# Performance work log

Measured on AMD Instinct MI355X. Metric: run time of the kernel, lower is better.

## Reference

```python
import jax, jax.numpy as jnp
import numpy as np

NEG = -1000000000.0

def _gru(x, h, W_ih, W_hh, b_ih, b_hh):
    # torch GRUCell semantics; W_ih: [3H, H_in], W_hh: [3H, H]
    gi = x @ W_ih.T + b_ih
    gh = h @ W_hh.T + b_hh
    i_r, i_z, i_n = jnp.split(gi, 3, axis=-1)
    h_r, h_z, h_n = jnp.split(gh, 3, axis=-1)
    r = jax.nn.sigmoid(i_r + h_r)
    z = jax.nn.sigmoid(i_z + h_z)
    n = jnp.tanh(i_n + r * h_n)
    return (1.0 - z) * n + z * h

def setup_inputs():
    key = jax.random.key(0)
    ks = jax.random.split(key, 32)
    N, E, ND, ED, H, P, L, M, S = 50000, 800000, 16, 16, 128, 16, 8, 6, 320
    sc = 0.05
    inp = {}
    inp['node_feat'] = jax.random.normal(ks[0], (N, ND), jnp.float32)
    inp['edge_feat'] = jax.random.normal(ks[1], (E, ED), jnp.float32)
    inp['edge_index'] = jax.random.randint(ks[2], (2, E), 0, N)
    inp['paths'] = jax.random.randint(ks[3], (P, L), 0, E)
    inp['path_mask'] = jnp.ones((P,), jnp.int32)
    inp['path_features'] = jax.random.normal(ks[4], (P, 3), jnp.float32)
    inp['mod_masks'] = jnp.ones((P, M), jnp.int32)
    inp['spec_masks'] = jnp.ones((P, M, S), jnp.int32)
    inp['path_spectrum'] = jax.random.uniform(ks[5], (P, S), jnp.float32)
    # parameters
    inp['W_np'] = jax.random.normal(ks[6], (ND, H), jnp.float32) * sc
    inp['b_np'] = jnp.zeros((H,), jnp.float32)
    inp['W_ep'] = jax.random.normal(ks[7], (ED, H), jnp.float32) * sc
    inp['b_ep'] = jnp.zeros((H,), jnp.float32)
    inp['W_msg'] = jax.random.normal(ks[8], (2 * H, H), jnp.float32) * sc
    inp['b_msg'] = jnp.zeros((H,), jnp.float32)
    inp['W_ih'] = jax.random.normal(ks[9], (3 * H, H), jnp.float32) * sc
    inp['b_ih'] = jnp.zeros((3 * H,), jnp.float32)
    inp['W_hh'] = jax.random.normal(ks[10], (3 * H, H), jnp.float32) * sc
    inp['b_hh'] = jnp.zeros((3 * H,), jnp.float32)
    inp['W_path'] = jax.random.normal(ks[11], (H, 1), jnp.float32) * sc
    inp['b_path'] = jnp.zeros((1,), jnp.float32)
    inp['W_mod'] = jax.random.normal(ks[12], (H + 3, M), jnp.float32) * sc
    inp['b_mod'] = jnp.zeros((M,), jnp.float32)
    inp['conv1_w'] = jax.random.normal(ks[13], (8, 1, 5), jnp.float32) * sc
    inp['conv1_b'] = jnp.zeros((8,), jnp.float32)
    inp['conv2_w'] = jax.random.normal(ks[14], (1, 8, 1), jnp.float32) * sc
    inp['conv2_b'] = jnp.zeros((1,), jnp.float32)
    inp['W_val'] = jax.random.normal(ks[15], (H, 1), jnp.float32) * sc
    inp['b_val'] = jnp.zeros((1,), jnp.float32)
    return inp

def reference(node_feat, edge_feat, edge_index, paths, path_mask, path_features,
              mod_masks, spec_masks, path_spectrum,
              W_np, b_np, W_ep, b_ep, W_msg, b_msg, W_ih, b_ih, W_hh, b_hh,
              W_path, b_path, W_mod, b_mod, conv1_w, conv1_b, conv2_w, conv2_b,
              W_val, b_val):
    N = node_feat.shape[0]
    # --- GNN encoder (3 iterations of gather -> message -> scatter -> GRU) ---
    h = node_feat @ W_np + b_np                       # [N, H]
    e = edge_feat @ W_ep + b_ep                       # [E, H]
    src, dst = edge_index[0], edge_index[1]
    for _ in range(3):
        m = jnp.concatenate([h[src], e], axis=-1) @ W_msg + b_msg   # [E, H]
        agg = jax.ops.segment_sum(m, dst, num_segments=N)           # index_add
        h = _gru(agg, h, W_ih, W_hh, b_ih, b_hh)
    # --- value head ---
    g = h.mean(axis=0)
    value = (g @ W_val + b_val).squeeze()
    # --- path agent (deterministic=True -> argmax) ---
    z = e[paths].mean(axis=1)                         # [P, H]
    logits_p = (z @ W_path + b_path).squeeze(-1)      # [P]
    logits_p = jnp.where(path_mask == 0, NEG, logits_p)
    p = jnp.argmax(logits_p)
    logp_p = jax.nn.log_softmax(logits_p)[p]
    z_p = z[p]
    # --- modulation agent ---
    x_m = jnp.concatenate([z_p, path_features[p]], axis=-1)
    logits_m = x_m @ W_mod + b_mod                    # [M]
    logits_m = jnp.where(mod_masks[p] == 0, NEG, logits_m)
    m_sel = jnp.argmax(logits_m)
    logp_m = jax.nn.log_softmax(logits_m)[m_sel]
    # --- spectrum agent ---
    spec = path_spectrum[p][None, None, :]            # [1,1,S]
    h1 = jax.nn.relu(jax.lax.conv_general_dilated(
        spec, conv1_w, (1,), [(2, 2)], dimension_numbers=('NCH', 'OIH', 'NCH'))
        + conv1_b[None, :, None])
    h2 = jax.lax.conv_general_dilated(
        h1, conv2_w, (1,), [(0, 0)], dimension_numbers=('NCH', 'OIH', 'NCH'))
    logits_f = h2.squeeze() + conv2_b[0]
    logits_f = jnp.where(spec_masks[p, m_sel] == 0, NEG, logits_f)
    f = jnp.argmax(logits_f)
    logp_f = jax.nn.log_softmax(logits_f)[f]
    logprob = logp_p + logp_m + logp_f
    return (p, f, m_sel, logprob, value)
```

## Files before the change

kernel.cpp:

```cpp
#include <hip/hip_runtime.h>
#include <math.h>

#define NN 50000
#define NE 800000
#define HD 128
#define FD 16
#define NPATH 16
#define PL 8
#define NM 6
#define NS 320
#define NB 196
#define NSB 782
#define AK 320
#define AKU 160
#define AK1 64
#define EPB 2048
#define NBLK 391
#define NBKT 196
#define NEGV -1000000000.0f

typedef unsigned int uint;
typedef unsigned short ushort;
typedef short bf16x8 __attribute__((ext_vector_type(8)));
typedef float f32x4 __attribute__((ext_vector_type(4)));

__device__ __forceinline__ float frcp(float x){ return __builtin_amdgcn_rcpf(x); }
__device__ __forceinline__ float fsigm(float x){ return frcp(1.0f + __expf(-x)); }
__device__ __forceinline__ float ftanh(float x){ return 1.0f - 2.0f*frcp(__expf(2.0f*x) + 1.0f); }

__device__ __forceinline__ ushort f2b(float f){
    union{float f; uint u;} v; v.f=f;
    uint r = v.u + 0x7FFFu + ((v.u>>16)&1u);
    return (ushort)(r>>16);
}
__device__ __forceinline__ float b2f(ushort s){
    union{uint u; float f;} v; v.u = ((uint)s)<<16; return v.f;
}
__device__ __forceinline__ float blo(uint v){ return b2f((ushort)(v&0xFFFF)); }
__device__ __forceinline__ float bhi(uint v){ return b2f((ushort)(v>>16)); }
__device__ __forceinline__ uint pack2(float a, float b){ return (uint)f2b(a) | (((uint)f2b(b))<<16); }

__global__ void k_deg(const int* __restrict__ ei, int* __restrict__ deg){
    int e = blockIdx.x*256 + threadIdx.x;
    if (e >= NE) return;
    atomicAdd(&deg[ei[NE + e]], 1);
}

__global__ void k_scan1(const int* __restrict__ deg, int* __restrict__ offs, int* __restrict__ bsum){
    int tid = threadIdx.x, bid = blockIdx.x;
    int idx = bid*256 + tid;
    int v = (idx<NN) ? deg[idx] : 0;
    int lane = tid&63, w = tid>>6;
    int x = v;
    #pragma unroll
    for (int d=1; d<64; d<<=1){ int y = __shfl_up(x,d); if (lane>=d) x += y; }
    __shared__ int wsum[4];
    if (lane==63) wsum[w] = x;
    __syncthreads();
    int base = 0;
    #pragma unroll
    for (int j=0;j<4;j++) if (j<w) base += wsum[j];
    if (idx<NN) offs[idx] = base + x - v;
    if (tid==255) bsum[bid] = base + x;
}
__global__ void k_scan2(int* __restrict__ bsum, int* __restrict__ offs){
    int tid = threadIdx.x;
    int v = (tid<NB) ? bsum[tid] : 0;
    int lane = tid&63, w = tid>>6;
    int x = v;
    #pragma unroll
    for (int d=1; d<64; d<<=1){ int y = __shfl_up(x,d); if (lane>=d) x += y; }
    __shared__ int wsum[4];
    if (lane==63) wsum[w] = x;
    __syncthreads();
    int base = 0;
    #pragma unroll
    for (int j=0;j<4;j++) if (j<w) base += wsum[j];
    if (tid<NB) bsum[tid] = base + x - v;
    if (tid==255) offs[NN] = base + x;
}
__global__ void k_scan3(const int* __restrict__ bsum, int* __restrict__ offs){
    int idx = blockIdx.x*256 + threadIdx.x;
    if (idx>=NN) return;
    offs[idx] += bsum[blockIdx.x];
}

__global__ void k_hist(const int* __restrict__ ei, int* __restrict__ C){
    __shared__ int h[NBKT];
    int tid = threadIdx.x, blk = blockIdx.x;
    if (tid < NBKT) h[tid] = 0;
    __syncthreads();
    int e0 = blk*EPB;
    for (int i=tid; i<EPB; i+=256){
        int e = e0+i;
        if (e < NE) atomicAdd(&h[ei[NE+e]>>8], 1);
    }
    __syncthreads();
    if (tid < NBKT) C[blk*NBKT + tid] = h[tid];
}

__global__ void k_cscan(int* __restrict__ C, const int* __restrict__ offs){
    int b = blockIdx.x*4 + (threadIdx.x>>6);
    int lane = threadIdx.x & 63;
    if (b >= NBKT) return;
    int base = offs[b<<8];
    int carry = 0;
    for (int c=0; c<7; ++c){
        int i = c*64 + lane;
        int v = (i<NBLK)? C[i*NBKT + b] : 0;
        int x = v;
        #pragma unroll
        for (int d=1; d<64; d<<=1){ int y = __shfl_up(x,d); if (lane>=d) x += y; }
        if (i<NBLK) C[i*NBKT + b] = base + carry + (x - v);
        carry += __shfl(x, 63);
    }
}

__global__ void k_scatA(const int* __restrict__ ei, const int* __restrict__ C,
                        int2* __restrict__ bkt2){
    __shared__ int cur[NBKT];
    __shared__ int cbase[NBKT];
    int tid = threadIdx.x, blk = blockIdx.x;
    if (tid < NBKT){ cur[tid] = 0; cbase[tid] = C[blk*NBKT + tid]; }
    __syncthreads();
    int e0 = blk*EPB;
    for (int i=tid; i<EPB; i+=256){
        int e = e0+i;
        if (e >= NE) break;
        int dst = ei[NE+e];
        int bkt = dst>>8;
        int r = atomicAdd(&cur[bkt], 1);
        bkt2[cbase[bkt] + r] = make_int2(dst, e);
    }
}

__global__ void k_scatB(const int* __restrict__ ei, const int2* __restrict__ bkt2,
                        const int* __restrict__ offs, int2* __restrict__ csr2){
    __shared__ int cur[256];
    int b = blockIdx.x, tid = threadIdx.x;
    int d0 = b<<8;
    {
        int idx = d0 + tid;
        cur[tid] = (idx<NN)? offs[idx] : 0;
    }
    __syncthreads();
    int lo = offs[d0];
    int hi = (d0+256 <= NN)? offs[d0+256] : offs[NN];
    for (int i=lo+tid; i<hi; i+=256){
        int2 p = bkt2[i];
        int pos = atomicAdd(&cur[p.x & 255], 1);
        csr2[pos] = make_int2(ei[p.y], p.y);
    }
}

__global__ void k_gat16(const int2* __restrict__ csr2,
                        const float* __restrict__ edge_feat, const float* __restrict__ nf,
                        const int* __restrict__ offs,
                        float* __restrict__ ef_sum, float* __restrict__ nf_sum){
    int node = blockIdx.x*4 + (threadIdx.x>>6);
    int lane = threadIdx.x & 63;
    int k = lane & 15, sub = lane >> 4;
    int b = offs[node], e2 = offs[node+1];
    float ae = 0.f, an = 0.f;
    int i = b + sub;
    for (; i + 4 < e2; i += 8){
        int2 p0 = csr2[i], p1 = csr2[i+4];
        float f0 = edge_feat[(size_t)p0.y*FD + k];
        float g0 = nf[(size_t)p0.x*FD + k];
        float f1 = edge_feat[(size_t)p1.y*FD + k];
        float g1 = nf[(size_t)p1.x*FD + k];
        ae += f0 + f1; an += g0 + g1;
    }
    if (i < e2){
        int2 p0 = csr2[i];
        ae += edge_feat[(size_t)p0.y*FD + k];
        an += nf[(size_t)p0.x*FD + k];
    }
    ae += __shfl_xor(ae, 16); ae += __shfl_xor(ae, 32);
    an += __shfl_xor(an, 16); an += __shfl_xor(an, 32);
    if (sub == 0){ ef_sum[node*FD + k] = ae; nf_sum[node*FD + k] = an; }
}

__global__ void k_folds(const float* __restrict__ W_ep, const float* __restrict__ b_ep,
                        const float* __restrict__ W_msg, const float* __restrict__ b_msg,
                        float* __restrict__ Wf, float* __restrict__ bfv){
    int o = blockIdx.x*256 + threadIdx.x;
    if (o < FD*HD){
        int k=o>>7, c=o&127;
        float acc=0.f;
        for (int m=0;m<HD;m++) acc += W_ep[k*HD+m]*W_msg[(HD+m)*HD+c];
        Wf[o]=acc;
    } else if (o < FD*HD+HD){
        int c=o-FD*HD;
        float acc=b_msg[c];
        for (int m=0;m<HD;m++) acc += b_ep[m]*W_msg[(HD+m)*HD+c];
        bfv[c]=acc;
    }
}

__global__ void k_wprep2(const float* __restrict__ W_ih, const float* __restrict__ W_hh,
                         const float* __restrict__ W_msg, const float* __restrict__ Wf,
                         const float* __restrict__ bfv,
                         const float* __restrict__ b_ih, const float* __restrict__ b_hh,
                         ushort* __restrict__ W2T, float* __restrict__ Wt32){
    int c = blockIdx.x;
    int k = threadIdx.x;
    int j = c>>2, g = c&3;
    float v = 0.f;
    if (k < 128){
        float acc = 0.f;
        if (g < 3){
            const float* wm = W_msg + (size_t)k*HD;
            const float* wi = W_ih + (size_t)(g*HD+j)*HD;
            for (int m=0;m<HD;m++) acc += wm[m]*wi[m];
        }
        Wt32[(size_t)c*HD + k] = acc;
        v = acc;
    } else if (k < 256){
        int kk = k-128;
        if (g==0)      v = W_hh[(size_t)j*HD+kk];
        else if (g==1) v = W_hh[(size_t)(HD+j)*HD+kk];
        else if (g==3) v = W_hh[(size_t)(2*HD+j)*HD+kk];
    } else if (k < 272){
        if (g < 3){
            const float* wf = Wf + (size_t)(k-256)*HD;
            const float* wi = W_ih + (size_t)(g*HD+j)*HD;
            float acc=0.f;
            for (int m=0;m<HD;m++) acc += wf[m]*wi[m];
            v = acc;
        }
    } else if (k == 272){
        if (g < 3){
            const float* wi = W_ih + (size_t)(g*HD+j)*HD;
            float acc=0.f;
            for (int m=0;m<HD;m++) acc += bfv[m]*wi[m];
            v = acc;
        }
    } else if (k == 273){
        v = (g==0)? b_ih[j]+b_hh[j] : (g==1)? b_ih[HD+j]+b_hh[HD+j]
          : (g==2)? b_ih[2*HD+j] : b_hh[2*HD+j];
    }
    W2T[(size_t)c*AK + k] = f2b(v);
}

__global__ void k_wprep1(const float* __restrict__ W_np, const float* __restrict__ b_np,
                         const float* __restrict__ W_hh, const float* __restrict__ Wt32,
                         const ushort* __restrict__ W2T, ushort* __restrict__ W1T){
    int c = blockIdx.x;
    int k = threadIdx.x;
    int j = c>>2, g = c&3;
    float v = 0.f;
    if (k < 16){
        if (g != 2){
            int gp = (g==3)? 2 : g;
            const float* wh = W_hh + (size_t)(gp*HD + j)*HD;
            const float* wn = W_np + (size_t)k*HD;
            float acc=0.f;
            for (int m=0;m<HD;m++) acc += wn[m]*wh[m];
            v = acc;
        }
    } else if (k < 32){
        const float* wt = Wt32 + (size_t)c*HD;
        const float* wn = W_np + (size_t)(k-16)*HD;
        float acc=0.f;
        for (int m=0;m<HD;m++) acc += wn[m]*wt[m];
        v = acc;
    } else if (k < 48){
        v = b2f(W2T[(size_t)c*AK + 256 + (k-32)]);
    } else if (k == 48){
        float acc = b2f(W2T[(size_t)c*AK + 272]);
        const float* wt = Wt32 + (size_t)c*HD;
        for (int m=0;m<HD;m++) acc += b_np[m]*wt[m];
        v = acc;
    } else if (k == 49){
        float acc = b2f(W2T[(size_t)c*AK + 273]);
        if (g != 2){
            int gp = (g==3)? 2 : g;
            const float* wh = W_hh + (size_t)(gp*HD + j)*HD;
            for (int m=0;m<HD;m++) acc += b_np[m]*wh[m];
        }
        v = acc;
    }
    W1T[(size_t)c*AK1 + k] = f2b(v);
}

__global__ void k_prep2(const float* __restrict__ nf, const float* __restrict__ nf_sum,
                        const float* __restrict__ ef_sum, const int* __restrict__ deg,
                        ushort* __restrict__ A1p, ushort* __restrict__ A){
    int idx = blockIdx.x*256 + threadIdx.x;
    int n = idx>>5, c2 = idx&31;
    int k = c2*2, k1 = k+1;
    float d = (float)deg[n];
    float v0 = (k<16)? nf[n*FD+k] : (k<32)? nf_sum[n*FD+k-16] : (k<48)? ef_sum[n*FD+k-32]
             : (k==48)? d : 0.f;
    float v1 = (k1<16)? nf[n*FD+k1] : (k1<32)? nf_sum[n*FD+k1-16] : (k1<48)? ef_sum[n*FD+k1-32]
             : (k1==49)? 1.f : 0.f;
    ((uint*)A1p)[(size_t)n*32 + c2] = pack2(v0,v1);
    int col = 256 + k;
    float s0 = (col<272)? ef_sum[n*FD + col-256] : (col==272)? d : 0.f;
    float s1 = (col+1<272)? ef_sum[n*FD + col+1-256] : (col+1==273)? 1.f : 0.f;
    ((uint*)A)[(size_t)n*AKU + 128 + c2] = pack2(s0,s1);
}

template<bool IT1>
__global__ __launch_bounds__(256) void k_fused(const ushort* __restrict__ Asrc,
                                               const ushort* __restrict__ Bt,
                                               const float* __restrict__ nf,
                                               const float* __restrict__ W_np,
                                               const float* __restrict__ b_np,
                                               ushort* __restrict__ Ah){
    __shared__ __align__(16) short LDS[128*128];
    __shared__ float Wnp_s[FD][32];
    short* As = LDS;
    short* Bs = LDS + 128*64;
    const int tid = threadIdx.x;
    const int lane = tid & 63, w = tid>>6;
    const int wm = w>>1, wn = w&1;
    const int n0 = blockIdx.x*128, m0 = blockIdx.y*128;
    const int jbase = n0>>2;
    const int AKA = IT1 ? AK1 : AK;
    if (IT1){
        for (int i=tid; i<FD*32; i+=256){
            int kk=i>>5, jj=i&31;
            Wnp_s[kk][jj] = W_np[kk*HD + jbase + jj];
        }
    }
    f32x4 acc[4][4] = {};
    const int nsteps = IT1 ? 1 : 5;
    for (int kk=0; kk<nsteps; ++kk){
        __syncthreads();
        #pragma unroll
        for (int i=0;i<4;i++){
            int id = tid + i*256;
            int row = id>>3, s = id&7;
            int phys = row*64 + ((s ^ (row&7))<<3);
            int ar = m0 + row; if (ar >= NN) ar = NN-1;
            *(int4*)&As[phys] = *(const int4*)(Asrc + (size_t)ar*AKA + kk*64 + s*8);
            *(int4*)&Bs[phys] = *(const int4*)(Bt + (size_t)(n0+row)*AKA + kk*64 + s*8);
        }
        __syncthreads();
        #pragma unroll
        for (int ksel=0; ksel<2; ++ksel){
            bf16x8 af[4], bfr[4];
            #pragma unroll
            for (int t=0;t<4;t++){
                int arow = wm*64 + t*16 + (lane&15);
                int aslot = (ksel*4 + (lane>>4)) ^ (arow&7);
                af[t] = *(const bf16x8*)&As[arow*64 + aslot*8];
                int brow = wn*64 + t*16 + (lane&15);
                int bslot = (ksel*4 + (lane>>4)) ^ (brow&7);
                bfr[t] = *(const bf16x8*)&Bs[brow*64 + bslot*8];
            }
            #pragma unroll
            for (int mi=0;mi<4;mi++)
                #pragma unroll
                for (int ni=0;ni<4;ni++)
                    acc[mi][ni] = __builtin_amdgcn_mfma_f32_16x16x32_bf16(af[mi], bfr[ni], acc[mi][ni], 0,0,0);
        }
    }
    __syncthreads();
    #pragma unroll
    for (int mi=0;mi<4;mi++){
        #pragma unroll
        for (int ni=0;ni<4;ni++){
            #pragma unroll
            for (int r=0;r<4;r++){
                int row = wm*64 + mi*16 + (lane>>4)*4 + r;
                int col = wn*64 + ni*16 + (lane&15);
                int pc = (col&3) | (((col>>2) ^ (row&7))<<2);
                LDS[row*128 + pc] = (short)f2b(acc[mi][ni][r]);
            }
        }
    }
    __syncthreads();
    {
        int jp = tid&15, rg = tid>>4;
        int jg = jbase + jp*2;
        #pragma unroll
        for (int rr=0; rr<8; ++rr){
            int row = rg*8 + rr;
            int n = m0 + row;
            if (n >= NN) continue;
            uint2 g0 = *(const uint2*)&LDS[row*128 + (((jp*2)   ^ (row&7))<<2)];
            uint2 g1 = *(const uint2*)&LDS[row*128 + (((jp*2+1) ^ (row&7))<<2)];
            float ha, hb;
            if constexpr (IT1){
                const float* x = nf + (size_t)n*FD;
                float a = b_np[jg], b = b_np[jg+1];
                #pragma unroll
                for (int k=0;k<FD;k++){
                    float xv = x[k];
                    a += xv*Wnp_s[k][jp*2];
                    b += xv*Wnp_s[k][jp*2+1];
                }
                ha = a; hb = b;
            } else {
                uint vh = ((const uint*)Ah)[(size_t)n*AKU + 64 + (n0>>3) + jp];
                ha = blo(vh); hb = bhi(vh);
            }
            float r0 = fsigm(blo(g0.x)), z0 = fsigm(bhi(g0.x));
            float nn0 = ftanh(blo(g0.y) + r0*bhi(g0.y));
            float r1 = fsigm(blo(g1.x)), z1 = fsigm(bhi(g1.x));
            float nn1 = ftanh(blo(g1.y) + r1*bhi(g1.y));
            float h0 = (1.f-z0)*nn0 + z0*ha;
            float h1 = (1.f-z1)*nn1 + z1*hb;
            ((uint*)Ah)[(size_t)n*AKU + 64 + (n0>>3) + jp] = pack2(h0,h1);
        }
    }
}

__global__ void k_gather(ushort* __restrict__ A, const int* __restrict__ offs,
                         const int2* __restrict__ csr2){
    int node = blockIdx.x*4 + (threadIdx.x>>6);
    int c2 = threadIdx.x & 63;
    int b = offs[node], e2 = offs[node+1];
    float a0 = 0.f, a1 = 0.f;
    const uint* hp = (const uint*)A;
    int i = b;
    for (; i + 8 <= e2; i += 8){
        int s0=csr2[i].x,  s1=csr2[i+1].x, s2=csr2[i+2].x, s3=csr2[i+3].x;
        int s4=csr2[i+4].x,s5=csr2[i+5].x, s6=csr2[i+6].x, s7=csr2[i+7].x;
        uint v0=hp[(size_t)s0*AKU+64+c2], v1=hp[(size_t)s1*AKU+64+c2],
             v2=hp[(size_t)s2*AKU+64+c2], v3=hp[(size_t)s3*AKU+64+c2],
             v4=hp[(size_t)s4*AKU+64+c2], v5=hp[(size_t)s5*AKU+64+c2],
             v6=hp[(size_t)s6*AKU+64+c2], v7=hp[(size_t)s7*AKU+64+c2];
        a0 += blo(v0)+blo(v1)+blo(v2)+blo(v3)+blo(v4)+blo(v5)+blo(v6)+blo(v7);
        a1 += bhi(v0)+bhi(v1)+bhi(v2)+bhi(v3)+bhi(v4)+bhi(v5)+bhi(v6)+bhi(v7);
    }
    if (i + 4 <= e2){
        int s0=csr2[i].x,s1=csr2[i+1].x,s2=csr2[i+2].x,s3=csr2[i+3].x;
        uint v0=hp[(size_t)s0*AKU+64+c2], v1=hp[(size_t)s1*AKU+64+c2],
             v2=hp[(size_t)s2*AKU+64+c2], v3=hp[(size_t)s3*AKU+64+c2];
        a0 += blo(v0)+blo(v1)+blo(v2)+blo(v3);
        a1 += bhi(v0)+bhi(v1)+bhi(v2)+bhi(v3);
        i += 4;
    }
    for (; i < e2; ++i){
        uint v = hp[(size_t)csr2[i].x*AKU+64+c2];
        a0 += blo(v); a1 += bhi(v);
    }
    ((uint*)A)[(size_t)node*AKU + c2] = pack2(a0,a1);
}

__global__ void k_sum1(const ushort* __restrict__ A, float* __restrict__ partial){
    int bid = blockIdx.x, tid = threadIdx.x;
    int lane = tid&63, w2 = tid>>6;
    int nb = bid*64;
    float a0=0.f, a1=0.f;
    const uint* hp = (const uint*)A;
    #pragma unroll
    for (int r=w2; r<64; r+=4){
        int n = nb + r;
        if (n < NN){
            uint v = hp[(size_t)n*AKU + 64 + lane];
            a0 += blo(v); a1 += bhi(v);
        }
    }
    __shared__ float s0[4][64], s1[4][64];
    s0[w2][lane]=a0; s1[w2][lane]=a1;
    __syncthreads();
    if (w2==0){
        a0 = s0[0][lane]+s0[1][lane]+s0[2][lane]+s0[3][lane];
        a1 = s1[0][lane]+s1[1][lane]+s1[2][lane]+s1[3][lane];
        ((float2*)partial)[(size_t)bid*64 + lane] = make_float2(a0,a1);
    }
}
__global__ void k_sum2(const float* __restrict__ partial, float* __restrict__ gsum){
    int c = blockIdx.x;
    int tid = threadIdx.x;
    int lane = tid&63, w = tid>>6;
    float a = 0.f;
    for (int b=tid; b<NSB; b+=256) a += partial[(size_t)b*128 + c];
    #pragma unroll
    for (int d=1; d<64; d<<=1) a += __shfl_xor(a, d);
    __shared__ float sh[4];
    if (lane==0) sh[w]=a;
    __syncthreads();
    if (tid==0) gsum[c] = sh[0]+sh[1]+sh[2]+sh[3];
}

__global__ void k_small(const float* __restrict__ ef, const int* __restrict__ paths,
                        const int* __restrict__ pmask, const float* __restrict__ pfeat,
                        const int* __restrict__ mmask, const int* __restrict__ smask,
                        const float* __restrict__ pspec,
                        const float* __restrict__ W_ep, const float* __restrict__ b_ep,
                        const float* __restrict__ W_path, const float* __restrict__ b_path,
                        const float* __restrict__ W_mod, const float* __restrict__ b_mod,
                        const float* __restrict__ c1w, const float* __restrict__ c1b,
                        const float* __restrict__ c2w, const float* __restrict__ c2b,
                        const float* __restrict__ W_val, const float* __restrict__ b_val,
                        const float* __restrict__ gsum, float* __restrict__ out){
    __shared__ float Wep_s[FD][HD];
    __shared__ float esum[NPATH][FD];
    __shared__ float z[NPATH][HD];
    __shared__ float lf[NS];
    __shared__ float spec[NS];
    __shared__ float red[8];
    __shared__ float scal[3];
    __shared__ int   sel[3];
    __shared__ float maxsh;
    int tid = threadIdx.x, lane = tid&63, w = tid>>6;

    for (int i=tid; i<FD*HD; i+=512) Wep_s[i>>7][i&127] = W_ep[i];
    if (tid < NPATH*FD){
        int p = tid>>4, k = tid&15;
        float a = 0.f;
        #pragma unroll
        for (int l=0;l<PL;l++){
            int eid = paths[p*PL + l];
            a += ef[(size_t)eid*FD + k];
        }
        esum[p][k] = a*0.125f;
    }
    __syncthreads();
    #pragma unroll
    for (int i=tid; i<NPATH*HD; i+=512){
        int p = i>>7, c = i&127;
        float a = b_ep[c];
        #pragma unroll
        for (int k=0;k<FD;k++) a += esum[p][k]*Wep_s[k][c];
        z[p][c] = a;
    }
    __syncthreads();
    {
        int p = tid>>5, sub = tid&31;
        float part = 0.f;
        #pragma unroll
        for (int c=sub;c<HD;c+=32) part += z[p][c]*W_path[c];
        #pragma unroll
        for (int d=16; d>=1; d>>=1) part += __shfl_xor(part, d);
        if (sub==0) lf[p] = (pmask[p]==0)? NEGV : part + b_path[0];
    }
    __syncthreads();
    if (w==0){
        float v = (lane<NPATH)? lf[lane] : -3.0e38f;
        float m = v;
        #pragma unroll
        for (int d=1; d<64; d<<=1) m = fmaxf(m, __shfl_xor(m, d));
        float e = (lane<NPATH)? __expf(v-m) : 0.f;
        #pragma unroll
        for (int d=1; d<64; d<<=1) e += __shfl_xor(e, d);
        int idx = (lane<NPATH && v==m)? lane : (1<<30);
        #pragma unroll
        for (int d=1; d<64; d<<=1) idx = min(idx, __shfl_xor(idx, d));
        if (lane==0){ sel[0]=idx; scal[0] = -logf(e); }
    }
    __syncthreads();
    int pstar = sel[0];
    if (w < NM){
        float part = 0.f;
        #pragma unroll
        for (int c=lane;c<HD;c+=64) part += z[pstar][c]*W_mod[c*NM + w];
        if (lane<3) part += pfeat[pstar*3+lane]*W_mod[(HD+lane)*NM + w];
        #pragma unroll
        for (int d=1; d<64; d<<=1) part += __shfl_xor(part, d);
        if (lane==0) red[w] = (mmask[pstar*NM + w]==0)? NEGV : part + b_mod[w];
    } else if (w == 7){
        float part = gsum[lane]*W_val[lane] + gsum[lane+64]*W_val[lane+64];
        #pragma unroll
        for (int d=1; d<64; d<<=1) part += __shfl_xor(part, d);
        if (lane==0) scal[2] = part/(float)NN + b_val[0];
    }
    __syncthreads();
    if (w==0){
        float v = (lane<NM)? red[lane] : -3.0e38f;
        float m = v;
        #pragma unroll
        for (int d=1; d<64; d<<=1) m = fmaxf(m, __shfl_xor(m, d));
        float e = (lane<NM)? __expf(v-m) : 0.f;
        #pragma unroll
        for (int d=1; d<64; d<<=1) e += __shfl_xor(e, d);
        int idx = (lane<NM && v==m)? lane : (1<<30);
        #pragma unroll
        for (int d=1; d<64; d<<=1) idx = min(idx, __shfl_xor(idx, d));
        if (lane==0){ sel[1]=idx; scal[1] = -logf(e); }
    }
    __syncthreads();
    int mstar = sel[1];
    if (tid < NS) spec[tid] = pspec[pstar*NS + tid];
    __syncthreads();
    float v = -3.0e38f;
    if (tid < NS){
        float acc = c2b[0];
        #pragma unroll
        for (int ch=0; ch<8; ch++){
            float a = c1b[ch];
            #pragma unroll
            for (int k=0;k<5;k++){
                int ss = tid + k - 2;
                if (ss>=0 && ss<NS) a += spec[ss]*c1w[ch*5+k];
            }
            a = fmaxf(a, 0.f);
            acc += a*c2w[ch];
        }
        v = (smask[pstar*NM*NS + mstar*NS + tid]==0) ? NEGV : acc;
    }
    float m = v;
    #pragma unroll
    for (int d=1; d<64; d<<=1) m = fmaxf(m, __shfl_xor(m, d));
    if (lane==0) red[w] = m;
    __syncthreads();
    if (tid==0){
        float mm = red[0];
        #pragma unroll
        for (int i=1;i<8;i++) mm = fmaxf(mm, red[i]);
        maxsh = mm; sel[2] = 1<<30;
    }
    __syncthreads();
    float M2 = maxsh;
    if (tid<NS && v==M2) atomicMin(&sel[2], tid);
    float e = (tid<NS)? __expf(v-M2) : 0.f;
    #pragma unroll
    for (int d=1; d<64; d<<=1) e += __shfl_xor(e, d);
    if (lane==0) red[w] = e;
    __syncthreads();
    if (tid==0){
        float se = 0.f;
        #pragma unroll
        for (int i=0;i<8;i++) se += red[i];
        out[0] = (float)pstar;
        out[1] = (float)sel[2];
        out[2] = (float)mstar;
        out[3] = scal[0] + scal[1] - logf(se);
        out[4] = scal[2];
    }
}

extern "C" void kernel_launch(void* const* d_in, const int* in_sizes, int n_in,
                              void* d_out, int out_size, void* d_ws, size_t ws_size,
                              hipStream_t stream) {
    (void)in_sizes; (void)n_in; (void)out_size; (void)ws_size;
    const float* node_feat     = (const float*)d_in[0];
    const float* edge_feat     = (const float*)d_in[1];
    const int*   edge_index    = (const int*)d_in[2];
    const int*   paths         = (const int*)d_in[3];
    const int*   path_mask     = (const int*)d_in[4];
    const float* path_features = (const float*)d_in[5];
    const int*   mod_masks     = (const int*)d_in[6];
    const int*   spec_masks    = (const int*)d_in[7];
    const float* path_spectrum = (const float*)d_in[8];
    const float* W_np  = (const float*)d_in[9];
    const float* b_np  = (const float*)d_in[10];
    const float* W_ep  = (const float*)d_in[11];
    const float* b_ep  = (const float*)d_in[12];
    const float* W_msg = (const float*)d_in[13];
    const float* b_msg = (const float*)d_in[14];
    const float* W_ih  = (const float*)d_in[15];
    const float* b_ih  = (const float*)d_in[16];
    const float* W_hh  = (const float*)d_in[17];
    const float* b_hh  = (const float*)d_in[18];
    const float* W_path = (const float*)d_in[19];
    const float* b_path = (const float*)d_in[20];
    const float* W_mod  = (const float*)d_in[21];
    const float* b_mod  = (const float*)d_in[22];
    const float* c1w = (const float*)d_in[23];
    const float* c1b = (const float*)d_in[24];
    const float* c2w = (const float*)d_in[25];
    const float* c2b = (const float*)d_in[26];
    const float* W_val = (const float*)d_in[27];
    const float* b_val = (const float*)d_in[28];

    char* ws = (char*)d_ws;
    size_t off = 0;
    auto alloc = [&](size_t bytes)->char*{
        char* p = ws + off;
        off += (bytes + 255) & ~(size_t)255;
        return p;
    };
    int*    deg     = (int*)alloc((size_t)NN*4);
    int*    offs    = (int*)alloc((size_t)(NN+1)*4);
    int*    bsum    = (int*)alloc((size_t)NB*4);
    int*    Cmat    = (int*)alloc((size_t)NBLK*NBKT*4);
    int2*   bkt2    = (int2*)alloc((size_t)NE*8);
    int2*   csr2    = (int2*)alloc((size_t)NE*8);
    float*  ef_sum  = (float*)alloc((size_t)NN*FD*4);
    float*  nf_sum  = (float*)alloc((size_t)NN*FD*4);
    float*  Wf      = (float*)alloc((size_t)FD*HD*4);
    float*  bfv     = (float*)alloc((size_t)HD*4);
    ushort* W2T     = (ushort*)alloc((size_t)512*AK*2);
    float*  Wt32    = (float*)alloc((size_t)512*HD*4);
    ushort* W1T     = (ushort*)alloc((size_t)512*AK1*2);
    ushort* A       = (ushort*)alloc((size_t)NN*AK*2);
    ushort* A1p     = (ushort*)alloc((size_t)NN*AK1*2);
    float*  partial = (float*)alloc((size_t)NSB*HD*4);
    float*  gsum    = (float*)alloc((size_t)HD*4);

    hipMemsetAsync(deg, 0, (size_t)NN*4, stream);

    k_deg<<<(NE+255)/256, 256, 0, stream>>>(edge_index, deg);
    k_scan1<<<NB, 256, 0, stream>>>(deg, offs, bsum);
    k_scan2<<<1, 256, 0, stream>>>(bsum, offs);
    k_scan3<<<NB, 256, 0, stream>>>(bsum, offs);
    k_hist<<<NBLK, 256, 0, stream>>>(edge_index, Cmat);
    k_cscan<<<(NBKT+3)/4, 256, 0, stream>>>(Cmat, offs);
    k_scatA<<<NBLK, 256, 0, stream>>>(edge_index, Cmat, bkt2);
    k_scatB<<<NBKT, 256, 0, stream>>>(edge_index, bkt2, offs, csr2);
    k_gat16<<<NN/4, 256, 0, stream>>>(csr2, edge_feat, node_feat, offs, ef_sum, nf_sum);
    k_folds<<<9, 256, 0, stream>>>(W_ep, b_ep, W_msg, b_msg, Wf, bfv);
    k_wprep2<<<512, AK, 0, stream>>>(W_ih, W_hh, W_msg, Wf, bfv, b_ih, b_hh, W2T, Wt32);
    k_wprep1<<<512, AK1, 0, stream>>>(W_np, b_np, W_hh, Wt32, W2T, W1T);
    k_prep2<<<NN*32/256, 256, 0, stream>>>(node_feat, nf_sum, ef_sum, deg, A1p, A);

    const int MB = (NN+127)/128;
    k_fused<true><<<dim3(4,MB), 256, 0, stream>>>(A1p, W1T, node_feat, W_np, b_np, A);
    k_gather<<<NN/4, 256, 0, stream>>>(A, offs, csr2);
    k_fused<false><<<dim3(4,MB), 256, 0, stream>>>(A, W2T, node_feat, W_np, b_np, A);
    k_gather<<<NN/4, 256, 0, stream>>>(A, offs, csr2);
    k_fused<false><<<dim3(4,MB), 256, 0, stream>>>(A, W2T, node_feat, W_np, b_np, A);

    k_sum1<<<NSB, 256, 0, stream>>>(A, partial);
    k_sum2<<<HD, 256, 0, stream>>>(partial, gsum);
    k_small<<<1, 512, 0, stream>>>(edge_feat, paths, path_mask, path_features,
                                   mod_masks, spec_masks, path_spectrum,
                                   W_ep, b_ep, W_path, b_path, W_mod, b_mod,
                                   c1w, c1b, c2w, c2b, W_val, b_val,
                                   gsum, (float*)d_out);
}
```

Before: 317.2 us.

## Derive CSR offsets from bucket sort, drop degree pass, remap GEMM blocks per XCD

```diff
diff --git a/kernel.cpp b/kernel.cpp
--- a/kernel.cpp
+++ b/kernel.cpp
@@ -1,4 +1,5 @@
 #include <hip/hip_runtime.h>
+#include <hip/hip_bf16.h>
 #include <math.h>
 
 #define NN 50000
@@ -9,7 +10,6 @@
 #define PL 8
 #define NM 6
 #define NS 320
-#define NB 196
 #define NSB 782
 #define AK 320
 #define AKU 160
@@ -17,6 +17,7 @@
 #define EPB 2048
 #define NBLK 391
 #define NBKT 196
+#define MBT 391
 #define NEGV -1000000000.0f
 
 typedef unsigned int uint;
@@ -29,9 +30,9 @@
 __device__ __forceinline__ float ftanh(float x){ return 1.0f - 2.0f*frcp(__expf(2.0f*x) + 1.0f); }
 
 __device__ __forceinline__ ushort f2b(float f){
-    union{float f; uint u;} v; v.f=f;
-    uint r = v.u + 0x7FFFu + ((v.u>>16)&1u);
-    return (ushort)(r>>16);
+    union { __hip_bfloat16 h; ushort u; } v;
+    v.h = __float2bfloat16(f);
+    return v.u;
 }
 __device__ __forceinline__ float b2f(ushort s){
     union{uint u; float f;} v; v.u = ((uint)s)<<16; return v.f;
@@ -39,51 +40,6 @@
 __device__ __forceinline__ float blo(uint v){ return b2f((ushort)(v&0xFFFF)); }
 __device__ __forceinline__ float bhi(uint v){ return b2f((ushort)(v>>16)); }
 __device__ __forceinline__ uint pack2(float a, float b){ return (uint)f2b(a) | (((uint)f2b(b))<<16); }
-
-__global__ void k_deg(const int* __restrict__ ei, int* __restrict__ deg){
-    int e = blockIdx.x*256 + threadIdx.x;
-    if (e >= NE) return;
-    atomicAdd(&deg[ei[NE + e]], 1);
-}
-
-__global__ void k_scan1(const int* __restrict__ deg, int* __restrict__ offs, int* __restrict__ bsum){
-    int tid = threadIdx.x, bid = blockIdx.x;
-    int idx = bid*256 + tid;
-    int v = (idx<NN) ? deg[idx] : 0;
-    int lane = tid&63, w = tid>>6;
-    int x = v;
-    #pragma unroll
-    for (int d=1; d<64; d<<=1){ int y = __shfl_up(x,d); if (lane>=d) x += y; }
-    __shared__ int wsum[4];
-    if (lane==63) wsum[w] = x;
-    __syncthreads();
-    int base = 0;
-    #pragma unroll
-    for (int j=0;j<4;j++) if (j<w) base += wsum[j];
-    if (idx<NN) offs[idx] = base + x - v;
-    if (tid==255) bsum[bid] = base + x;
-}
-__global__ void k_scan2(int* __restrict__ bsum, int* __restrict__ offs){
-    int tid = threadIdx.x;
-    int v = (tid<NB) ? bsum[tid] : 0;
-    int lane = tid&63, w = tid>>6;
-    int x = v;
-    #pragma unroll
-    for (int d=1; d<64; d<<=1){ int y = __shfl_up(x,d); if (lane>=d) x += y; }
-    __shared__ int wsum[4];
-    if (lane==63) wsum[w] = x;
-    __syncthreads();
-    int base = 0;
-    #pragma unroll
-    for (int j=0;j<4;j++) if (j<w) base += wsum[j];
-    if (tid<NB) bsum[tid] = base + x - v;
-    if (tid==255) offs[NN] = base + x;
-}
-__global__ void k_scan3(const int* __restrict__ bsum, int* __restrict__ offs){
-    int idx = blockIdx.x*256 + threadIdx.x;
-    if (idx>=NN) return;
-    offs[idx] += bsum[blockIdx.x];
-}
 
 __global__ void k_hist(const int* __restrict__ ei, int* __restrict__ C){
     __shared__ int h[NBKT];
@@ -99,11 +55,10 @@
     if (tid < NBKT) C[blk*NBKT + tid] = h[tid];
 }
 
-__global__ void k_cscan(int* __restrict__ C, const int* __restrict__ offs){
+__global__ void k_cscanA(int* __restrict__ C, int* __restrict__ bkttot){
     int b = blockIdx.x*4 + (threadIdx.x>>6);
     int lane = threadIdx.x & 63;
     if (b >= NBKT) return;
-    int base = offs[b<<8];
     int carry = 0;
     for (int c=0; c<7; ++c){
         int i = c*64 + lane;
@@ -111,17 +66,36 @@
         int x = v;
         #pragma unroll
         for (int d=1; d<64; d<<=1){ int y = __shfl_up(x,d); if (lane>=d) x += y; }
-        if (i<NBLK) C[i*NBKT + b] = base + carry + (x - v);
+        if (i<NBLK) C[i*NBKT + b] = carry + (x - v);
         carry += __shfl(x, 63);
     }
+    if (lane==0) bkttot[b] = carry;
+}
+
+__global__ void k_bscan(const int* __restrict__ bkttot, int* __restrict__ bktbase,
+                        int* __restrict__ offs){
+    int tid = threadIdx.x, lane = tid&63, w = tid>>6;
+    int v = (tid<NBKT)? bkttot[tid] : 0;
+    int x = v;
+    #pragma unroll
+    for (int d=1; d<64; d<<=1){ int y = __shfl_up(x,d); if (lane>=d) x += y; }
+    __shared__ int wsum[4];
+    if (lane==63) wsum[w] = x;
+    __syncthreads();
+    int base = 0;
+    #pragma unroll
+    for (int j=0;j<4;j++) if (j<w) base += wsum[j];
+    int excl = base + x - v;
+    if (tid < NBKT) bktbase[tid] = excl;
+    if (tid == NBKT){ bktbase[NBKT] = excl; offs[NN] = excl; }
 }
 
 __global__ void k_scatA(const int* __restrict__ ei, const int* __restrict__ C,
-                        int2* __restrict__ bkt2){
+                        const int* __restrict__ bktbase, int2* __restrict__ bkt2){
     __shared__ int cur[NBKT];
     __shared__ int cbase[NBKT];
     int tid = threadIdx.x, blk = blockIdx.x;
-    if (tid < NBKT){ cur[tid] = 0; cbase[tid] = C[blk*NBKT + tid]; }
+    if (tid < NBKT){ cur[tid] = 0; cbase[tid] = bktbase[tid] + C[blk*NBKT + tid]; }
     __syncthreads();
     int e0 = blk*EPB;
     for (int i=tid; i<EPB; i+=256){
@@ -135,17 +109,30 @@
 }
 
 __global__ void k_scatB(const int* __restrict__ ei, const int2* __restrict__ bkt2,
-                        const int* __restrict__ offs, int2* __restrict__ csr2){
+                        const int* __restrict__ bktbase,
+                        int* __restrict__ offs, int2* __restrict__ csr2){
+    __shared__ int cnt[256];
     __shared__ int cur[256];
-    int b = blockIdx.x, tid = threadIdx.x;
+    __shared__ int wsum[4];
+    int b = blockIdx.x, tid = threadIdx.x, lane = tid&63, w = tid>>6;
     int d0 = b<<8;
-    {
-        int idx = d0 + tid;
-        cur[tid] = (idx<NN)? offs[idx] : 0;
-    }
-    __syncthreads();
-    int lo = offs[d0];
-    int hi = (d0+256 <= NN)? offs[d0+256] : offs[NN];
+    cnt[tid] = 0;
+    __syncthreads();
+    int lo = bktbase[b], hi = bktbase[b+1];
+    for (int i=lo+tid; i<hi; i+=256) atomicAdd(&cnt[bkt2[i].x & 255], 1);
+    __syncthreads();
+    int v = cnt[tid], x = v;
+    #pragma unroll
+    for (int d=1; d<64; d<<=1){ int y = __shfl_up(x,d); if (lane>=d) x += y; }
+    if (lane==63) wsum[w] = x;
+    __syncthreads();
+    int base = 0;
+    #pragma unroll
+    for (int j=0;j<4;j++) if (j<w) base += wsum[j];
+    int o = lo + base + x - v;
+    if (d0+tid < NN) offs[d0+tid] = o;
+    cur[tid] = o;
+    __syncthreads();
     for (int i=lo+tid; i<hi; i+=256){
         int2 p = bkt2[i];
         int pos = atomicAdd(&cur[p.x & 255], 1);
@@ -285,12 +272,12 @@
 }
 
 __global__ void k_prep2(const float* __restrict__ nf, const float* __restrict__ nf_sum,
-                        const float* __restrict__ ef_sum, const int* __restrict__ deg,
+                        const float* __restrict__ ef_sum, const int* __restrict__ offs,
                         ushort* __restrict__ A1p, ushort* __restrict__ A){
     int idx = blockIdx.x*256 + threadIdx.x;
     int n = idx>>5, c2 = idx&31;
     int k = c2*2, k1 = k+1;
-    float d = (float)deg[n];
+    float d = (float)(offs[n+1] - offs[n]);
     float v0 = (k<16)? nf[n*FD+k] : (k<32)? nf_sum[n*FD+k-16] : (k<48)? ef_sum[n*FD+k-32]
              : (k==48)? d : 0.f;
     float v1 = (k1<16)? nf[n*FD+k1] : (k1<32)? nf_sum[n*FD+k1-16] : (k1<48)? ef_sum[n*FD+k1-32]
@@ -310,21 +297,20 @@
                                                const float* __restrict__ b_np,
                                                ushort* __restrict__ Ah){
     __shared__ __align__(16) short LDS[128*128];
-    __shared__ float Wnp_s[FD][32];
     short* As = LDS;
     short* Bs = LDS + 128*64;
+    const int bid = blockIdx.x;
+    const int xcd = bid & 7;
+    const int t = bid >> 3;
+    const int gb = t & 3;
+    const int mt = xcd + ((t >> 2) << 3);
+    if (mt >= MBT) return;
     const int tid = threadIdx.x;
     const int lane = tid & 63, w = tid>>6;
     const int wm = w>>1, wn = w&1;
-    const int n0 = blockIdx.x*128, m0 = blockIdx.y*128;
+    const int n0 = gb*128, m0 = mt*128;
     const int jbase = n0>>2;
     const int AKA = IT1 ? AK1 : AK;
-    if (IT1){
-        for (int i=tid; i<FD*32; i+=256){
-            int kk=i>>5, jj=i&31;
-            Wnp_s[kk][jj] = W_np[kk*HD + jbase + jj];
-        }
-    }
     f32x4 acc[4][4] = {};
     const int nsteps = IT1 ? 1 : 5;
     for (int kk=0; kk<nsteps; ++kk){
@@ -343,13 +329,13 @@
         for (int ksel=0; ksel<2; ++ksel){
             bf16x8 af[4], bfr[4];
             #pragma unroll
-            for (int t=0;t<4;t++){
-                int arow = wm*64 + t*16 + (lane&15);
+            for (int t2=0;t2<4;t2++){
+                int arow = wm*64 + t2*16 + (lane&15);
                 int aslot = (ksel*4 + (lane>>4)) ^ (arow&7);
-                af[t] = *(const bf16x8*)&As[arow*64 + aslot*8];
-                int brow = wn*64 + t*16 + (lane&15);
+                af[t2] = *(const bf16x8*)&As[arow*64 + aslot*8];
+                int brow = wn*64 + t2*16 + (lane&15);
                 int bslot = (ksel*4 + (lane>>4)) ^ (brow&7);
-                bfr[t] = *(const bf16x8*)&Bs[brow*64 + bslot*8];
+                bfr[t2] = *(const bf16x8*)&Bs[brow*64 + bslot*8];
             }
             #pragma unroll
             for (int mi=0;mi<4;mi++)
@@ -390,8 +376,8 @@
                 #pragma unroll
                 for (int k=0;k<FD;k++){
                     float xv = x[k];
-                    a += xv*Wnp_s[k][jp*2];
-                    b += xv*Wnp_s[k][jp*2+1];
+                    a += xv*W_np[k*HD + jg];
+                    b += xv*W_np[k*HD + jg + 1];
                 }
                 ha = a; hb = b;
             } else {
@@ -667,10 +653,10 @@
         off += (bytes + 255) & ~(size_t)255;
         return p;
     };
-    int*    deg     = (int*)alloc((size_t)NN*4);
     int*    offs    = (int*)alloc((size_t)(NN+1)*4);
-    int*    bsum    = (int*)alloc((size_t)NB*4);
     int*    Cmat    = (int*)alloc((size_t)NBLK*NBKT*4);
+    int*    bkttot  = (int*)alloc((size_t)NBKT*4);
+    int*    bktbase = (int*)alloc((size_t)(NBKT+1)*4);
     int2*   bkt2    = (int2*)alloc((size_t)NE*8);
     int2*   csr2    = (int2*)alloc((size_t)NE*8);
     float*  ef_sum  = (float*)alloc((size_t)NN*FD*4);
@@ -685,28 +671,23 @@
     float*  partial = (float*)alloc((size_t)NSB*HD*4);
     float*  gsum    = (float*)alloc((size_t)HD*4);
 
-    hipMemsetAsync(deg, 0, (size_t)NN*4, stream);
-
-    k_deg<<<(NE+255)/256, 256, 0, stream>>>(edge_index, deg);
-    k_scan1<<<NB, 256, 0, stream>>>(deg, offs, bsum);
-    k_scan2<<<1, 256, 0, stream>>>(bsum, offs);
-    k_scan3<<<NB, 256, 0, stream>>>(bsum, offs);
     k_hist<<<NBLK, 256, 0, stream>>>(edge_index, Cmat);
-    k_cscan<<<(NBKT+3)/4, 256, 0, stream>>>(Cmat, offs);
-    k_scatA<<<NBLK, 256, 0, stream>>>(edge_index, Cmat, bkt2);
-    k_scatB<<<NBKT, 256, 0, stream>>>(edge_index, bkt2, offs, csr2);
+    k_cscanA<<<(NBKT+3)/4, 256, 0, stream>>>(Cmat, bkttot);
+    k_bscan<<<1, 256, 0, stream>>>(bkttot, bktbase, offs);
+    k_scatA<<<NBLK, 256, 0, stream>>>(edge_index, Cmat, bktbase, bkt2);
+    k_scatB<<<NBKT, 256, 0, stream>>>(edge_index, bkt2, bktbase, offs, csr2);
     k_gat16<<<NN/4, 256, 0, stream>>>(csr2, edge_feat, node_feat, offs, ef_sum, nf_sum);
     k_folds<<<9, 256, 0, stream>>>(W_ep, b_ep, W_msg, b_msg, Wf, bfv);
     k_wprep2<<<512, AK, 0, stream>>>(W_ih, W_hh, W_msg, Wf, bfv, b_ih, b_hh, W2T, Wt32);
     k_wprep1<<<512, AK1, 0, stream>>>(W_np, b_np, W_hh, Wt32, W2T, W1T);
-    k_prep2<<<NN*32/256, 256, 0, stream>>>(node_feat, nf_sum, ef_sum, deg, A1p, A);
-
-    const int MB = (NN+127)/128;
-    k_fused<true><<<dim3(4,MB), 256, 0, stream>>>(A1p, W1T, node_feat, W_np, b_np, A);
+    k_prep2<<<NN*32/256, 256, 0, stream>>>(node_feat, nf_sum, ef_sum, offs, A1p, A);
+
+    const int GRID = 8*4*49;
+    k_fused<true><<<GRID, 256, 0, stream>>>(A1p, W1T, node_feat, W_np, b_np, A);
     k_gather<<<NN/4, 256, 0, stream>>>(A, offs, csr2);
-    k_fused<false><<<dim3(4,MB), 256, 0, stream>>>(A, W2T, node_feat, W_np, b_np, A);
+    k_fused<false><<<GRID, 256, 0, stream>>>(A, W2T, node_feat, W_np, b_np, A);
     k_gather<<<NN/4, 256, 0, stream>>>(A, offs, csr2);
-    k_fused<false><<<dim3(4,MB), 256, 0, stream>>>(A, W2T, node_feat, W_np, b_np, A);
+    k_fused<false><<<GRID, 256, 0, stream>>>(A, W2T, node_feat, W_np, b_np, A);
 
     k_sum1<<<NSB, 256, 0, stream>>>(A, partial);
     k_sum2<<<HD, 256, 0, stream>>>(partial, gsum);
```

Result: faster. 295.7 us (-6.8%).
